# Performance work log

Hardware: AMD Instinct MI355X
Metric: run time of the kernel (lower is better)

The kernel has to match this reference:

```python
import jax, jax.numpy as jnp
import numpy as np

EMB = 1024
NH = 8
HD = EMB // NH
EPS = 1e-6


def setup_inputs() -> dict:
    key = jax.random.key(0)
    ks = jax.random.split(key, 6)
    B, S = 2, 2048
    q = jax.random.normal(ks[0], (B, S, EMB), jnp.float32)
    k = jax.random.normal(ks[1], (B, S, EMB), jnp.float32)
    v = jax.random.normal(ks[2], (B, S, EMB), jnp.float32)
    # gate Dense params: input dim 3*EMB (concat of q,k,v), output NH
    igate_kernel = jax.random.normal(ks[3], (3 * EMB, NH), jnp.float32) * 0.02
    igate_bias = jax.random.normal(ks[4], (NH,), jnp.float32) * 0.1
    fgate_kernel = jax.random.normal(ks[5], (3 * EMB, NH), jnp.float32) * 0.02
    fgate_bias = jnp.linspace(3.0, 6.0, NH).astype(jnp.float32)  # bias_linspace_init
    return dict(q=q, k=k, v=v, igate_kernel=igate_kernel, igate_bias=igate_bias,
                fgate_kernel=fgate_kernel, fgate_bias=fgate_bias)


def _mlstm_head(q, k, v, ig, fg):
    # q,k,v: (S, DH); ig, fg: (S, 1) gate preactivations for this head
    S, DH = q.shape
    log_fg = jax.nn.log_sigmoid(fg)                                   # (S,1)
    cs = jnp.concatenate([jnp.zeros((1, 1), q.dtype),
                          jnp.cumsum(log_fg, axis=0)], axis=0)        # (S+1,1)
    fg_mat_full = cs - cs.T                                           # (S+1,S+1): cumsum_i - cumsum_j
    ltr = jnp.tril(jnp.ones((S, S), bool))
    log_fg_matrix = jnp.where(ltr, fg_mat_full[1:, 1:], -jnp.inf)     # causal decay
    log_D = log_fg_matrix + ig.T                                      # (S,S)
    max_log_D = jnp.max(log_D, axis=-1, keepdims=True)                # row-wise stabilizer
    D = jnp.exp(log_D - max_log_D)
    qk = q @ (k.T / jnp.sqrt(jnp.asarray(DH, q.dtype)))               # (S,S)
    C = qk * D
    normalizer = jnp.maximum(jnp.abs(C.sum(-1, keepdims=True)), jnp.exp(-max_log_D))
    return (C / (normalizer + EPS)) @ v                               # (S,DH)


def reference(q, k, v, igate_kernel, igate_bias, fgate_kernel, fgate_bias):
    B, S, H = q.shape
    x = jnp.concatenate([q, k, v], axis=-1)                           # (B,S,3H)
    ig = x @ igate_kernel + igate_bias                                # (B,S,NH)
    fg = x @ fgate_kernel + fgate_bias                                # (B,S,NH)
    qh = q.reshape(B, S, NH, HD).swapaxes(1, 2)                       # (B,NH,S,DH)
    kh = k.reshape(B, S, NH, HD).swapaxes(1, 2)
    vh = v.reshape(B, S, NH, HD).swapaxes(1, 2)
    igp = ig.swapaxes(1, 2)[..., None]                                # (B,NH,S,1)
    fgp = fg.swapaxes(1, 2)[..., None]
    h = jax.vmap(jax.vmap(_mlstm_head))(qh, kh, vh, igp, fgp)         # (B,NH,S,DH)
    # RMSNorm over head_dim (last axis), computed in fp32
    hf = h.astype(jnp.float32)
    h = (hf * jax.lax.rsqrt(jnp.mean(jnp.square(hf), axis=-1, keepdims=True) + 1e-6)).astype(h.dtype)
    return h.swapaxes(1, 2).reshape(B, S, H)
```

## Files before the change

kernel.cpp:

```cpp
#include <hip/hip_runtime.h>

#define S_LEN 2048
#define EMB_D 1024
#define QK_SCALE 0.08838834764831845f
#define RS128 11.313708498984761f
#define LOG2E 1.4426950408889634f

typedef _Float16 f16;
typedef f16 f16x8 __attribute__((ext_vector_type(8)));
typedef float f32x4 __attribute__((ext_vector_type(4)));
typedef unsigned short ushort_t;

typedef const __attribute__((address_space(1))) void gvoid;
typedef __attribute__((address_space(3))) void lvoid;

__device__ __forceinline__ ushort_t f2h(float x) {
    return __builtin_bit_cast(ushort_t, (f16)x);
}
__device__ __forceinline__ unsigned pk2h(float a, float b) {
    return __builtin_bit_cast(unsigned, __builtin_amdgcn_cvt_pkrtz(a, b));
}
__device__ __forceinline__ void gl_lds(const void* g, void* l) {
    __builtin_amdgcn_global_load_lds((gvoid*)g, (lvoid*)l, 16, 0, 0);
}

__global__ __launch_bounds__(256) void ktransW(const float* __restrict__ igk,
                                               const float* __restrict__ fgk,
                                               ushort_t* __restrict__ Wf) {
    int gid = blockIdx.x * 256 + threadIdx.x;
    int ks_g = gid >> 6, lane = gid & 63;
    int n = lane & 15, lg = lane >> 4;
    int src = ks_g >> 5, rem = ks_g & 31;
    int hemb = rem >> 2, ks = rem & 3;
    int e0 = src * 1024 + hemb * 128 + ks * 32 + lg * 8;
    float scale = (src == 0) ? RS128 : 1.0f;
    const float* col = (n < 8) ? igk : fgk;
    int nn = n & 7;
    union { ushort_t u[8]; uint4 v4; } P;
    #pragma unroll
    for (int e = 0; e < 8; ++e) P.u[e] = f2h(col[(size_t)(e0 + e) * 8 + nn] * scale);
    *(uint4*)((char*)Wf + ks_g * 1024 + lane * 16) = P.v4;
}

__global__ __launch_bounds__(256) void kprep(const float* __restrict__ q,
                                             const float* __restrict__ k,
                                             const float* __restrict__ v,
                                             const ushort_t* __restrict__ Wf,
                                             const float* __restrict__ igb,
                                             const float* __restrict__ fgb,
                                             ushort_t* __restrict__ Qf,
                                             ushort_t* __restrict__ Kf,
                                             ushort_t* __restrict__ Vt,
                                             float* __restrict__ igp_t,
                                             float* __restrict__ fgp_t) {
    __shared__ __align__(16) ushort_t xs[3 * 8 * 16 * 128];
    __shared__ __align__(16) float red[4][64][4];
    const int blk = blockIdx.x;
    const int b = blk >> 7, strip = blk & 127;
    const int s0 = strip * 16;
    const int tile = strip >> 2, subrow = (strip & 3) * 16;
    const int t = threadIdx.x;
    const int w = t >> 6, lane = t & 63;
    const int ll = lane & 15, lg = lane >> 4;

    #pragma unroll
    for (int src = 0; src < 3; ++src) {
        const float* sp = (src == 0 ? q : src == 1 ? k : v) + ((size_t)b * S_LEN + s0) * EMB_D;
        float scale = (src == 0) ? QK_SCALE : 1.0f;
        #pragma unroll
        for (int i = 0; i < 16; ++i) {
            int f = i * 256 + t;
            int r = f >> 8, c4 = f & 255;
            int col = c4 * 4;
            float4 x = *(const float4*)(sp + (size_t)r * EMB_D + col);
            ushort4 H;
            H.x = f2h(x.x * scale); H.y = f2h(x.y * scale);
            H.z = f2h(x.z * scale); H.w = f2h(x.w * scale);
            int hh = col >> 7, d0 = col & 127;
            *(ushort4*)((char*)xs + ((((src * 8 + hh) * 16 + r) * 256 + d0 * 2) ^ ((r & 7) << 4))) = H;
            if (src < 2) {
                char* dst = (char*)(src ? Kf : Qf) + ((size_t)(b * 8 + hh) * 32 + tile) * 16384;
                *(ushort4*)(dst + (((subrow + r) * 256 + d0 * 2) ^ ((r & 7) << 4))) = H;
            }
        }
    }
    __syncthreads();
    #pragma unroll
    for (int it = 0; it < 8; ++it) {
        int item = it * 256 + t;
        int d = item & 127, jo = (item >> 7) & 1, hh = item >> 8;
        union { ushort_t u[8]; uint4 v4; } P;
        #pragma unroll
        for (int e = 0; e < 8; ++e) {
            int r = jo * 8 + e;
            P.u[e] = *(const ushort_t*)((const char*)xs
                       + ((((16 + hh) * 16 + r) * 256 + d * 2) ^ ((r & 7) << 4)));
        }
        char* vd = (char*)Vt + ((size_t)(b * 8 + hh) * 32 + tile) * 16384
                 + ((strip & 3) * 2 + jo) * 2048 + d * 16;
        *(uint4*)vd = P.v4;
    }
    f32x4 acc = {0.f, 0.f, 0.f, 0.f};
    for (int ri = w * 6; ri < w * 6 + 6; ++ri) {
        int src = ri >> 3, hemb = ri & 7;
        #pragma unroll
        for (int ks = 0; ks < 4; ++ks) {
            f16x8 af = *(const f16x8*)((const char*)xs
                        + ((((src * 8 + hemb) * 16 + ll) * 256 + ks * 64 + lg * 16) ^ ((ll & 7) << 4)));
            f16x8 bf = *(const f16x8*)((const char*)Wf + (src * 32 + hemb * 4 + ks) * 1024 + lane * 16);
            acc = __builtin_amdgcn_mfma_f32_16x16x32_f16(af, bf, acc, 0, 0, 0);
        }
    }
    *(f32x4*)&red[w][lane][0] = acc;
    __syncthreads();
    if (w == 0) {
        f32x4 o2 = acc;
        #pragma unroll
        for (int ww = 1; ww < 4; ++ww) o2 += *(const f32x4*)&red[ww][lane][0];
        float bias = (ll < 8) ? igb[ll] : fgb[ll - 8];
        float* dst = (ll < 8) ? igp_t : fgp_t;
        size_t ob = (size_t)(b * 8 + (ll & 7)) * S_LEN + s0 + lg * 4;
        #pragma unroll
        for (int r = 0; r < 4; ++r) dst[ob + r] = o2[r] + bias;
    }
}

__global__ __launch_bounds__(64) void kscan(const float* __restrict__ igp_t,
                                            const float* __restrict__ fgp_t,
                                            float* __restrict__ a_w,
                                            float* __restrict__ pm_w,
                                            float* __restrict__ nf_w) {
    const int bh = blockIdx.x;
    const int l = threadIdx.x;
    const int base = bh * S_LEN + l * 32;
    float lf[32];
    #pragma unroll
    for (int i = 0; i < 8; ++i) {
        float4 fg = *(const float4*)(fgp_t + base + i * 4);
        float* p = &lf[i * 4];
        p[0] = fminf(fg.x, 0.f) - log1pf(__expf(-fabsf(fg.x)));
        p[1] = fminf(fg.y, 0.f) - log1pf(__expf(-fabsf(fg.y)));
        p[2] = fminf(fg.z, 0.f) - log1pf(__expf(-fabsf(fg.z)));
        p[3] = fminf(fg.w, 0.f) - log1pf(__expf(-fabsf(fg.w)));
    }
    #pragma unroll
    for (int i = 1; i < 32; ++i) lf[i] += lf[i - 1];
    float tot = lf[31];
    #pragma unroll
    for (int d = 1; d < 64; d <<= 1) {
        float n = __shfl_up(tot, d, 64);
        if (l >= d) tot += n;
    }
    float excl = tot - lf[31];
    float cs[32], a[32];
    #pragma unroll
    for (int i = 0; i < 8; ++i) {
        float4 ig = *(const float4*)(igp_t + base + i * 4);
        float iv[4] = {ig.x, ig.y, ig.z, ig.w};
        #pragma unroll
        for (int e = 0; e < 4; ++e) {
            int idx = i * 4 + e;
            cs[idx] = excl + lf[idx];
            a[idx] = iv[e] - cs[idx];
            a_w[base + idx] = a[idx] * LOG2E;
        }
    }
    float am[32];
    am[0] = a[0];
    #pragma unroll
    for (int i = 1; i < 32; ++i) am[i] = fmaxf(am[i - 1], a[i]);
    float mtot = am[31];
    #pragma unroll
    for (int d = 1; d < 64; d <<= 1) {
        float n = __shfl_up(mtot, d, 64);
        if (l >= d) mtot = fmaxf(mtot, n);
    }
    float exm = __shfl_up(mtot, 1, 64);
    if (l == 0) exm = -INFINITY;
    #pragma unroll
    for (int i = 0; i < 32; ++i) {
        float pmv = fmaxf(exm, am[i]);
        pm_w[base + i] = pmv * LOG2E;
        nf_w[base + i] = __expf(-(cs[i] + pmv));
    }
}

__global__ __launch_bounds__(512) void kmain(const ushort_t* __restrict__ Qf,
                                             const ushort_t* __restrict__ Kf,
                                             const ushort_t* __restrict__ Vt,
                                             const float* __restrict__ a_w,
                                             const float* __restrict__ pm_w,
                                             const float* __restrict__ nf_w,
                                             float* __restrict__ out) {
    __shared__ __align__(16) ushort_t Kbuf[2][2][8192];
    __shared__ __align__(16) ushort_t Vbuf[2][2][8192];
    __shared__ __align__(16) ushort_t Csh[2][4096];
    __shared__ float redL[2][2][64];

    const int blk = blockIdx.x;
    const int bh = blk & 15;
    const int pair = blk >> 4;
    const int b = bh >> 3, h = bh & 7;
    const int t = threadIdx.x;
    const int w = t >> 6, lane = t & 63;
    const int g = w >> 2, wl = w & 3;
    const int wr = wl >> 1, wc = wl & 1;
    const int lg = lane >> 4, ll = lane & 15;
    const int sw = (ll & 7) << 4;

    const char* q_b = (const char*)Qf + (size_t)bh * 524288;
    const char* k_b = (const char*)Kf + (size_t)bh * 524288;
    const char* v_b = (const char*)Vt + (size_t)bh * 524288;
    const float* aw = a_w + bh * S_LEN;

    float* accX = (float*)&Kbuf[0][0][0];
    float* rsX  = (float*)&Csh[0][0];

    for (int half = 0; half < 2; ++half) {
        const int rt = half ? (31 - pair) : pair;
        const int row0 = rt * 64;
        const int nss = (rt >> 1) + 1;
        __syncthreads();

        const char* qt = q_b + (size_t)rt * 16384;
        f16x8 qf[2][4];
        #pragma unroll
        for (int ib = 0; ib < 2; ++ib) {
            int row = 32 * wr + 16 * ib + ll;
            #pragma unroll
            for (int kk = 0; kk < 4; ++kk)
                qf[ib][kk] = *(const f16x8*)(qt + ((row * 256 + lg * 16 + kk * 64) ^ ((row & 7) << 4)));
        }
        float pm2[2];
        #pragma unroll
        for (int ib = 0; ib < 2; ++ib)
            pm2[ib] = pm_w[bh * S_LEN + row0 + 32 * wr + 16 * ib + ll];

        f32x4 avA[2] = {{0.f,0.f,0.f,0.f},{0.f,0.f,0.f,0.f}};
        f32x4 avB[2] = {{0.f,0.f,0.f,0.f},{0.f,0.f,0.f,0.f}};
        if (g <= rt) {
            const char* kt = k_b + (size_t)g * 16384;
            const char* vt = v_b + (size_t)g * 16384;
            #pragma unroll
            for (int i = 0; i < 4; ++i) {
                int o = (wl * 4 + i) * 1024 + lane * 16;
                gl_lds(kt + o, (char*)&Kbuf[g][0][0] + o);
                gl_lds(vt + o, (char*)&Vbuf[g][0][0] + o);
            }
            #pragma unroll
            for (int jb = 0; jb < 2; ++jb)
                avA[jb] = *(const f32x4*)(aw + g * 64 + 32 * wc + 16 * jb + 4 * lg);
        }
        asm volatile("s_waitcnt vmcnt(0)" ::: "memory");
        __builtin_amdgcn_s_barrier();

        f32x4 zero4 = {0.f, 0.f, 0.f, 0.f};
        f32x4 accO[2][4];
        #pragma unroll
        for (int ib = 0; ib < 2; ++ib)
            #pragma unroll
            for (int vf = 0; vf < 4; ++vf) accO[ib][vf] = zero4;
        float rs[2] = {0.f, 0.f};

        for (int ss = 0; ss < nss; ++ss) {
            const int p = ss & 1;
            const int myct = 2 * ss + g;
            const int nxct = myct + 2;
            if (nxct <= rt) {
                const char* kt = k_b + (size_t)nxct * 16384;
                const char* vt = v_b + (size_t)nxct * 16384;
                #pragma unroll
                for (int i = 0; i < 4; ++i) {
                    int o = (wl * 4 + i) * 1024 + lane * 16;
                    gl_lds(kt + o, (char*)&Kbuf[g][p ^ 1][0] + o);
                    gl_lds(vt + o, (char*)&Vbuf[g][p ^ 1][0] + o);
                }
                if (p == 0) {
                    #pragma unroll
                    for (int jb = 0; jb < 2; ++jb)
                        avB[jb] = *(const f32x4*)(aw + nxct * 64 + 32 * wc + 16 * jb + 4 * lg);
                } else {
                    #pragma unroll
                    for (int jb = 0; jb < 2; ++jb)
                        avA[jb] = *(const f32x4*)(aw + nxct * 64 + 32 * wc + 16 * jb + 4 * lg);
                }
            }
            const bool act = (myct <= rt);
            if (act) {
                const char* kl = (const char*)&Kbuf[g][p][0];
                f32x4 accST[2][2];
                accST[0][0] = zero4; accST[0][1] = zero4;
                accST[1][0] = zero4; accST[1][1] = zero4;
                __builtin_amdgcn_s_setprio(1);
                #pragma unroll
                for (int kk = 0; kk < 4; ++kk) {
                    f16x8 kf0 = *(const f16x8*)(kl + (((32 * wc + ll) * 256 + lg * 16 + kk * 64) ^ sw));
                    f16x8 kf1 = *(const f16x8*)(kl + (((32 * wc + 16 + ll) * 256 + lg * 16 + kk * 64) ^ sw));
                    accST[0][0] = __builtin_amdgcn_mfma_f32_16x16x32_f16(kf0, qf[0][kk], accST[0][0], 0, 0, 0);
                    accST[0][1] = __builtin_amdgcn_mfma_f32_16x16x32_f16(kf0, qf[1][kk], accST[0][1], 0, 0, 0);
                    accST[1][0] = __builtin_amdgcn_mfma_f32_16x16x32_f16(kf1, qf[0][kk], accST[1][0], 0, 0, 0);
                    accST[1][1] = __builtin_amdgcn_mfma_f32_16x16x32_f16(kf1, qf[1][kk], accST[1][1], 0, 0, 0);
                }
                __builtin_amdgcn_s_setprio(0);
                const bool diag = (myct == rt);
                #pragma unroll
                for (int jb = 0; jb < 2; ++jb) {
                    f32x4 av;
                    #pragma unroll
                    for (int r = 0; r < 4; ++r) av[r] = (p == 0) ? avA[jb][r] : avB[jb][r];
                    #pragma unroll
                    for (int ib = 0; ib < 2; ++ib) {
                        int il = 32 * wr + 16 * ib + ll;
                        float cv[4];
                        #pragma unroll
                        for (int r = 0; r < 4; ++r) {
                            int jl = 32 * wc + 16 * jb + 4 * lg + r;
                            float x = accST[jb][ib][r] * exp2f(av[r] - pm2[ib]);
                            if (diag && jl > il) x = 0.f;
                            rs[ib] += x;
                            cv[r] = x;
                        }
                        int off = (il * 128 + (32 * wc + 16 * jb + 4 * lg) * 2) ^ ((il & 7) << 4);
                        uint2 pk2; pk2.x = pk2h(cv[0], cv[1]); pk2.y = pk2h(cv[2], cv[3]);
                        *(uint2*)((char*)&Csh[g][0] + off) = pk2;
                    }
                }
            }
            asm volatile("s_waitcnt lgkmcnt(0)" ::: "memory");
            __builtin_amdgcn_s_barrier();
            if (act) {
                const char* vl = (const char*)&Vbuf[g][p][0];
                __builtin_amdgcn_s_setprio(1);
                #pragma unroll
                for (int kk = 0; kk < 2; ++kk)
                    #pragma unroll
                    for (int ib = 0; ib < 2; ++ib) {
                        int rowA = 32 * wr + 16 * ib + ll;
                        f16x8 pa = *(const f16x8*)((const char*)&Csh[g][0]
                                                   + ((rowA * 128 + lg * 16 + kk * 64) ^ ((rowA & 7) << 4)));
                        #pragma unroll
                        for (int vf = 0; vf < 4; ++vf) {
                            f16x8 vb2 = *(const f16x8*)(vl + (kk * 4 + lg) * 2048
                                                        + (64 * wc + 16 * vf + ll) * 16);
                            accO[ib][vf] = __builtin_amdgcn_mfma_f32_16x16x32_f16(pa, vb2, accO[ib][vf], 0, 0, 0);
                        }
                    }
                __builtin_amdgcn_s_setprio(0);
            }
            asm volatile("s_waitcnt vmcnt(0)" ::: "memory");
            __builtin_amdgcn_s_barrier();
        }

        __syncthreads();
        const int li = wl * 64 + lane;
        const int lsw = (li & 7) << 2;
        if (g == 1) {
            #pragma unroll
            for (int ib = 0; ib < 2; ++ib)
                #pragma unroll
                for (int vf = 0; vf < 4; ++vf)
                    *(f32x4*)&accX[(li * 32 + (ib * 4 + vf) * 4) ^ lsw] = accO[ib][vf];
            rsX[li * 2 + 0] = rs[0];
            rsX[li * 2 + 1] = rs[1];
        }
        __syncthreads();
        if (g == 0) {
            #pragma unroll
            for (int ib = 0; ib < 2; ++ib)
                #pragma unroll
                for (int vf = 0; vf < 4; ++vf)
                    accO[ib][vf] += *(const f32x4*)&accX[(li * 32 + (ib * 4 + vf) * 4) ^ lsw];
            rs[0] += rsX[li * 2 + 0];
            rs[1] += rsX[li * 2 + 1];
            #pragma unroll
            for (int ib = 0; ib < 2; ++ib) {
                rs[ib] += __shfl_xor(rs[ib], 16);
                rs[ib] += __shfl_xor(rs[ib], 32);
            }
            if (lg == 0) {
                redL[0][wc][32 * wr + ll] = rs[0];
                redL[0][wc][32 * wr + 16 + ll] = rs[1];
            }
        }
        __syncthreads();
        if (g == 0) {
            float invn[2][4];
            #pragma unroll
            for (int ib = 0; ib < 2; ++ib)
                #pragma unroll
                for (int r = 0; r < 4; ++r) {
                    int il = 32 * wr + 16 * ib + 4 * lg + r;
                    float tot = redL[0][0][il] + redL[0][1][il];
                    float nf = nf_w[bh * S_LEN + row0 + il];
                    invn[ib][r] = 1.0f / (fmaxf(fabsf(tot), nf) + 1e-6f);
                }
            float ssq[2][4] = {{0.f, 0.f, 0.f, 0.f}, {0.f, 0.f, 0.f, 0.f}};
            #pragma unroll
            for (int ib = 0; ib < 2; ++ib)
                #pragma unroll
                for (int vf = 0; vf < 4; ++vf)
                    #pragma unroll
                    for (int r = 0; r < 4; ++r) {
                        float hv = accO[ib][vf][r] * invn[ib][r];
                        ssq[ib][r] += hv * hv;
                    }
            #pragma unroll
            for (int m = 1; m < 16; m <<= 1)
                #pragma unroll
                for (int ib = 0; ib < 2; ++ib)
                    #pragma unroll
                    for (int r = 0; r < 4; ++r) ssq[ib][r] += __shfl_xor(ssq[ib][r], m);
            if (ll == 0) {
                #pragma unroll
                for (int ib = 0; ib < 2; ++ib)
                    #pragma unroll
                    for (int r = 0; r < 4; ++r)
                        redL[1][wc][32 * wr + 16 * ib + 4 * lg + r] = ssq[ib][r];
            }
            __builtin_amdgcn_s_barrier();
            float* ob = out + ((size_t)b * S_LEN + row0) * EMB_D + h * 128;
            #pragma unroll
            for (int ib = 0; ib < 2; ++ib)
                #pragma unroll
                for (int r = 0; r < 4; ++r) {
                    int il = 32 * wr + 16 * ib + 4 * lg + r;
                    float sst = redL[1][0][il] + redL[1][1][il];
                    float scl = rsqrtf(sst * (1.0f / 128.0f) + 1e-6f) * invn[ib][r];
                    #pragma unroll
                    for (int vf = 0; vf < 4; ++vf) {
                        int d = 64 * wc + 16 * vf + ll;
                        ob[(size_t)il * EMB_D + d] = accO[ib][vf][r] * scl;
                    }
                }
        } else {
            __builtin_amdgcn_s_barrier();
        }
    }
}

extern "C" void kernel_launch(void* const* d_in, const int* in_sizes, int n_in,
                              void* d_out, int out_size, void* d_ws, size_t ws_size,
                              hipStream_t stream) {
    const float* q   = (const float*)d_in[0];
    const float* k   = (const float*)d_in[1];
    const float* v   = (const float*)d_in[2];
    const float* igk = (const float*)d_in[3];
    const float* igb = (const float*)d_in[4];
    const float* fgk = (const float*)d_in[5];
    const float* fgb = (const float*)d_in[6];
    float* out = (float*)d_out;

    char* W = (char*)d_ws;
    ushort_t* Wf   = (ushort_t*)(W);
    float* igp_t   = (float*)(W + 98304);
    float* fgp_t   = (float*)(W + 229376);
    float* a_w     = (float*)(W + 360448);
    float* pm_w    = (float*)(W + 491520);
    float* nf_w    = (float*)(W + 622592);
    ushort_t* Qf   = (ushort_t*)(W + 753664);
    ushort_t* Kf   = (ushort_t*)(W + 753664 + 1 * 8388608ull);
    ushort_t* Vt   = (ushort_t*)(W + 753664 + 2 * 8388608ull);

    ktransW<<<24, 256, 0, stream>>>(igk, fgk, Wf);
    kprep<<<256, 256, 0, stream>>>(q, k, v, Wf, igb, fgb, Qf, Kf, Vt, igp_t, fgp_t);
    kscan<<<16, 64, 0, stream>>>(igp_t, fgp_t, a_w, pm_w, nf_w);
    kmain<<<256, 512, 0, stream>>>(Qf, Kf, Vt, a_w, pm_w, nf_w, out);
}
```

Before: 77.80 us.

## Stagger QK and PV phases between warp groups with a single barrier per step

Restructures the main loop so the two warp groups run offset by one phase: while one group does its QK^T MFMA and decay-mask step, the other does its PV MFMA. Each step now has one barrier instead of two, and each group runs only as many tiles as it owns. The aim is to cut barrier stalls and let the two MFMA phases overlap across groups. In exchange the loop needs more steps, the per-step predicate logic is more complex, and the waitcnt placement depends on which phase a group is in.

```diff
diff --git a/kernel.cpp b/kernel.cpp
--- a/kernel.cpp
+++ b/kernel.cpp
@@ -219,7 +219,10 @@
     for (int half = 0; half < 2; ++half) {
         const int rt = half ? (31 - pair) : pair;
         const int row0 = rt * 64;
-        const int nss = (rt >> 1) + 1;
+        const int T0h = (rt >> 1) + 1;
+        const int T1h = (rt >= 1) ? (((rt - 1) >> 1) + 1) : 0;
+        const int Tg  = g ? T1h : T0h;
+        const int Nint = (2 * T1h + 1 > 2 * T0h) ? (2 * T1h + 1) : (2 * T0h);
         __syncthreads();
 
         const char* qt = q_b + (size_t)rt * 16384;
@@ -238,7 +241,7 @@
 
         f32x4 avA[2] = {{0.f,0.f,0.f,0.f},{0.f,0.f,0.f,0.f}};
         f32x4 avB[2] = {{0.f,0.f,0.f,0.f},{0.f,0.f,0.f,0.f}};
-        if (g <= rt) {
+        if (Tg > 0) {
             const char* kt = k_b + (size_t)g * 16384;
             const char* vt = v_b + (size_t)g * 16384;
             #pragma unroll
@@ -262,32 +265,35 @@
             for (int vf = 0; vf < 4; ++vf) accO[ib][vf] = zero4;
         float rs[2] = {0.f, 0.f};
 
-        for (int ss = 0; ss < nss; ++ss) {
-            const int p = ss & 1;
-            const int myct = 2 * ss + g;
-            const int nxct = myct + 2;
-            if (nxct <= rt) {
-                const char* kt = k_b + (size_t)nxct * 16384;
-                const char* vt = v_b + (size_t)nxct * 16384;
-                #pragma unroll
-                for (int i = 0; i < 4; ++i) {
-                    int o = (wl * 4 + i) * 1024 + lane * 16;
-                    gl_lds(kt + o, (char*)&Kbuf[g][p ^ 1][0] + o);
-                    gl_lds(vt + o, (char*)&Vbuf[g][p ^ 1][0] + o);
+        for (int i = 0; i < Nint; ++i) {
+            const int d = i - g;
+            const bool isQK = (d >= 0) && ((d & 1) == 0) && ((d >> 1) < Tg);
+            const bool isPV = (d >= 1) && ((d & 1) == 1) && (((d - 1) >> 1) < Tg);
+            if (isQK) {
+                const int tt = d >> 1;
+                const int ct = 2 * tt + g;
+                if (tt + 1 < Tg) {
+                    const int nct = ct + 2;
+                    const char* kt = k_b + (size_t)nct * 16384;
+                    const char* vt = v_b + (size_t)nct * 16384;
+                    const int pn = (tt + 1) & 1;
+                    #pragma unroll
+                    for (int ii = 0; ii < 4; ++ii) {
+                        int o = (wl * 4 + ii) * 1024 + lane * 16;
+                        gl_lds(kt + o, (char*)&Kbuf[g][pn][0] + o);
+                        gl_lds(vt + o, (char*)&Vbuf[g][pn][0] + o);
+                    }
+                    if ((tt + 1) & 1) {
+                        #pragma unroll
+                        for (int jb = 0; jb < 2; ++jb)
+                            avB[jb] = *(const f32x4*)(aw + nct * 64 + 32 * wc + 16 * jb + 4 * lg);
+                    } else {
+                        #pragma unroll
+                        for (int jb = 0; jb < 2; ++jb)
+                            avA[jb] = *(const f32x4*)(aw + nct * 64 + 32 * wc + 16 * jb + 4 * lg);
+                    }
                 }
-                if (p == 0) {
-                    #pragma unroll
-                    for (int jb = 0; jb < 2; ++jb)
-                        avB[jb] = *(const f32x4*)(aw + nxct * 64 + 32 * wc + 16 * jb + 4 * lg);
-                } else {
-                    #pragma unroll
-                    for (int jb = 0; jb < 2; ++jb)
-                        avA[jb] = *(const f32x4*)(aw + nxct * 64 + 32 * wc + 16 * jb + 4 * lg);
-                }
-            }
-            const bool act = (myct <= rt);
-            if (act) {
-                const char* kl = (const char*)&Kbuf[g][p][0];
+                const char* kl = (const char*)&Kbuf[g][tt & 1][0];
                 f32x4 accST[2][2];
                 accST[0][0] = zero4; accST[0][1] = zero4;
                 accST[1][0] = zero4; accST[1][1] = zero4;
@@ -302,12 +308,12 @@
                     accST[1][1] = __builtin_amdgcn_mfma_f32_16x16x32_f16(kf1, qf[1][kk], accST[1][1], 0, 0, 0);
                 }
                 __builtin_amdgcn_s_setprio(0);
-                const bool diag = (myct == rt);
+                const bool diag = (ct == rt);
                 #pragma unroll
                 for (int jb = 0; jb < 2; ++jb) {
                     f32x4 av;
                     #pragma unroll
-                    for (int r = 0; r < 4; ++r) av[r] = (p == 0) ? avA[jb][r] : avB[jb][r];
+                    for (int r = 0; r < 4; ++r) av[r] = (tt & 1) ? avB[jb][r] : avA[jb][r];
                     #pragma unroll
                     for (int ib = 0; ib < 2; ++ib) {
                         int il = 32 * wr + 16 * ib + ll;
@@ -325,11 +331,11 @@
                         *(uint2*)((char*)&Csh[g][0] + off) = pk2;
                     }
                 }
-            }
-            asm volatile("s_waitcnt lgkmcnt(0)" ::: "memory");
-            __builtin_amdgcn_s_barrier();
-            if (act) {
-                const char* vl = (const char*)&Vbuf[g][p][0];
+                asm volatile("s_waitcnt lgkmcnt(0)" ::: "memory");
+            }
+            if (isPV) {
+                const int tp = (d - 1) >> 1;
+                const char* vl = (const char*)&Vbuf[g][tp & 1][0];
                 __builtin_amdgcn_s_setprio(1);
                 #pragma unroll
                 for (int kk = 0; kk < 2; ++kk)
@@ -346,8 +352,8 @@
                         }
                     }
                 __builtin_amdgcn_s_setprio(0);
-            }
-            asm volatile("s_waitcnt vmcnt(0)" ::: "memory");
+                asm volatile("s_waitcnt vmcnt(0)" ::: "memory");
+            }
             __builtin_amdgcn_s_barrier();
         }
 
@@ -428,8 +434,8 @@
                     float scl = rsqrtf(sst * (1.0f / 128.0f) + 1e-6f) * invn[ib][r];
                     #pragma unroll
                     for (int vf = 0; vf < 4; ++vf) {
-                        int d = 64 * wc + 16 * vf + ll;
-                        ob[(size_t)il * EMB_D + d] = accO[ib][vf][r] * scl;
+                        int d2 = 64 * wc + 16 * vf + ll;
+                        ob[(size_t)il * EMB_D + d2] = accO[ib][vf][r] * scl;
                     }
                 }
         } else {
```

Result: slower. 90.76 us (+16.7%).
